# Kernel tuning notes

Measured on AMD Instinct MI355X. Metric: run time of the kernel, lower is better.

Reference implementation:

```python
import jax, jax.numpy as jnp
import numpy as np

EPS = 1e-12  # matches F.normalize default eps


def _l2norm(a, axis):
    n = jnp.sqrt(jnp.sum(a * a, axis=axis, keepdims=True))
    return a / jnp.maximum(n, EPS)


def setup_inputs() -> dict:
    key = jax.random.key(0)
    k1, k2, k3, k4, k5 = jax.random.split(key, 5)
    B, H, W = 512, 64, 64
    Y, Z = 32768, 1000
    x = jax.random.normal(k1, (B, H, W), dtype=jnp.float32)
    z = jax.random.randint(k2, (B,), 0, Z, dtype=jnp.int64 if jax.config.jax_enable_x64 else jnp.int32).astype(jnp.int32)
    x2y_w = jax.random.uniform(k3, (Y, H * W), dtype=jnp.float32)
    y2z_w = jax.random.uniform(k4, (Z, Y), dtype=jnp.float32)
    y_age = jax.random.randint(k5, (1, Y), 0, 3, dtype=jnp.int32)
    return {"x": x, "z": z, "x2y_w": x2y_w, "y2z_w": y2z_w, "y_age": y_age, "per_item": 1}


def reference(x, z, x2y_w, y2z_w, y_age, per_item):
    # DN.forward, mode='test'
    B = x.shape[0]
    Y = x2y_w.shape[0]
    xf = _l2norm(x.reshape(B, -1), axis=1)              # [B, X]
    w_xy = _l2norm(x2y_w, axis=1)                       # row-normalized [Y, X]
    w_yz = _l2norm(y2z_w, axis=1)                       # row-normalized [Z, Y]
    y_bu = jnp.einsum('bx,yx->by', xf, w_xy)            # bottom-up response [B, Y]
    active = (y_age >= 1).astype(y_bu.dtype)            # [1, Y] age gate
    y_pre = y_bu * active                               # gated responses
    # top_k_competition(flag=0): top-1 winner-take-all -> one-hot response
    winner = jnp.argmax(y_pre, axis=1)                  # [B]
    y_resp = jax.nn.one_hot(winner, Y, dtype=y_pre.dtype)  # [B, Y]
    out = jnp.einsum('by,zy->bz', y_resp, w_yz)         # [B, Z]
    return out
```

## Files before the change

### kernel.cpp

```cpp
#include <hip/hip_runtime.h>
#include <math.h>


typedef _Float16 half8 __attribute__((ext_vector_type(8)));
typedef __attribute__((ext_vector_type(16))) float f32x16;
typedef unsigned long long ull;

#define TAU 0.006f
#define CAP 1572864u
#define LCAP 1536u

__device__ __forceinline__ unsigned pk2h(float a, float b) {
    union { _Float16 h; unsigned short u; } ca, cb;
    ca.h = (_Float16)a; cb.h = (_Float16)b;
    return (unsigned)ca.u | ((unsigned)cb.u << 16);
}

__device__ __forceinline__ ull packkey(float v, unsigned y) {
    unsigned m = __float_as_uint(v);
    m = (v >= 0.f) ? (m | 0x80000000u) : ~m;
    return ((ull)m << 32) | (ull)(0x7FFFFFFFu - y);
}

__global__ __launch_bounds__(512) void init_ctrl(const int* __restrict__ age,
                                                 ull* __restrict__ win,
                                                 unsigned* __restrict__ cnt) {
    const int t = threadIdx.x;
    int fi = 0x7fffffff;
    for (int y = t; y < 32768; y += 512)
        if (age[y] < 1) fi = min(fi, y);
    __shared__ int red[512];
    red[t] = fi;
    __syncthreads();
    for (int s = 256; s; s >>= 1) {
        if (t < s) red[t] = min(red[t], red[t + s]);
        __syncthreads();
    }
    const int f = red[0];
    const ull seed = (f < 32768) ? packkey(0.0f, (unsigned)f) : packkey(-1e30f, 0u);
    win[t] = seed;
    if (t == 0) *cnt = 0u;
}

__global__ __launch_bounds__(512) void convert_x(const float* __restrict__ x,
                                                 uint4* __restrict__ xf16) {
    const int o = blockIdx.x * 512 + threadIdx.x;
    const int lane = o & 63;
    const int ks = (o >> 6) & 1;
    const int mi = (o >> 7) & 1;
    const int wm = (o >> 8) & 7;
    const int t  = o >> 11;
    const int row = (wm << 6) + (mi << 5) + (lane & 31);
    const int col = (t << 5) + (ks << 4) + ((lane >> 5) << 3);
    const float* src = x + (size_t)row * 4096 + col;
    const float4 a = *(const float4*)src;
    const float4 b = *(const float4*)(src + 4);
    uint4 u;
    u.x = pk2h(a.x, a.y); u.y = pk2h(a.z, a.w);
    u.z = pk2h(b.x, b.y); u.w = pk2h(b.z, b.w);
    xf16[o] = u;
}

__global__ __launch_bounds__(256) void row_norms(const float* __restrict__ src,
                                                 float* __restrict__ dst, int cols) {
    const int r = blockIdx.x;
    const float* row = src + (size_t)r * cols;
    const int t = threadIdx.x;
    float s = 0.f;
    const int nIter = cols >> 10;
    for (int i = 0; i < nIter; ++i) {
        const float4 v = *reinterpret_cast<const float4*>(row + (((i << 8) + t) << 2));
        s = fmaf(v.x, v.x, s); s = fmaf(v.y, v.y, s);
        s = fmaf(v.z, v.z, s); s = fmaf(v.w, v.w, s);
    }
    #pragma unroll
    for (int off = 32; off; off >>= 1) s += __shfl_down(s, off);
    __shared__ float red[4];
    if ((t & 63) == 0) red[t >> 6] = s;
    __syncthreads();
    if (t == 0) dst[r] = sqrtf(red[0] + red[1] + red[2] + red[3]);
}

__global__ __launch_bounds__(512, 2) void gemm_f16(
    const float* __restrict__ w,
    const uint4* __restrict__ xf16,
    const int*  __restrict__ age,
    float* __restrict__ cand,
    float2* __restrict__ ent,
    unsigned* __restrict__ cnt)
{
    __shared__ uint4 Bl[4][512];
    __shared__ float ny_inv[128];
    __shared__ float rowmaxs[512];
    __shared__ float2 lent[LCAP];
    __shared__ unsigned lcnt, gbase;

    const int tid = threadIdx.x;
    const int y0 = blockIdx.x << 7;

    const int rB = tid >> 2, q = tid & 3;
    const int wiB = (rB << 2) + (q ^ (rB & 3));
    const float* bP = w + (size_t)(y0 + rB) * 4096 + (q << 3);

    const int lane = tid & 63, wm = tid >> 6;
    const int kh = lane >> 5, cc = lane & 3;
    const uint4* aP = xf16 + (wm << 8) + lane;

    const int rb0 = ((lane & 31)      ) << 2;
    const int rb1 = ((lane & 31) +  32) << 2;
    const int rb2 = ((lane & 31) +  64) << 2;
    const int rb3 = ((lane & 31) +  96) << 2;
    const int s0 = kh ^ cc, s1 = (2 | kh) ^ cc;

    f32x16 am0n0 = (f32x16)0.f, am0n1 = (f32x16)0.f;
    f32x16 am0n2 = (f32x16)0.f, am0n3 = (f32x16)0.f;
    f32x16 am1n0 = (f32x16)0.f, am1n1 = (f32x16)0.f;
    f32x16 am1n2 = (f32x16)0.f, am1n3 = (f32x16)0.f;

    half8 pa00, pa01, pa10, pa11;
    half8 qa00, qa01, qa10, qa11;
    half8 g00, g10, g20, g30;
    half8 g01, g11, g21, g31;
    float4 SAa, SAb, SBa, SBb;
    float4 SCa, SCb, SDa, SDb;
    float nyacc = 0.f;

#define MF(a, b, c) __builtin_amdgcn_mfma_f32_32x32x16_f16(a, b, c, 0, 0, 0)
#define LG0 asm volatile("s_waitcnt lgkmcnt(0)" ::: "memory")
#define SBR __builtin_amdgcn_sched_barrier(0)

#define LOADA(S, tt) { const uint4* p_ = aP + ((size_t)(tt) << 11); \
    S##00 = *(const half8*)(p_);        S##01 = *(const half8*)(p_ + 64); \
    S##10 = *(const half8*)(p_ + 128);  S##11 = *(const half8*)(p_ + 192); }

#define LOADW(S, tt) { const float* p_ = bP + ((tt) << 5); \
    S##a = *(const float4*)p_; S##b = *(const float4*)(p_ + 4); }

#define STOREB(buf, S) { uint4 u_; \
    u_.x = pk2h(S##a.x, S##a.y); u_.y = pk2h(S##a.z, S##a.w); \
    u_.z = pk2h(S##b.x, S##b.y); u_.w = pk2h(S##b.z, S##b.w); \
    Bl[buf][wiB] = u_; \
    nyacc = fmaf(S##a.x, S##a.x, nyacc); nyacc = fmaf(S##a.y, S##a.y, nyacc); \
    nyacc = fmaf(S##a.z, S##a.z, nyacc); nyacc = fmaf(S##a.w, S##a.w, nyacc); \
    nyacc = fmaf(S##b.x, S##b.x, nyacc); nyacc = fmaf(S##b.y, S##b.y, nyacc); \
    nyacc = fmaf(S##b.z, S##b.z, nyacc); nyacc = fmaf(S##b.w, S##b.w, nyacc); }

#define LDB(cur) { \
    g00 = *(const half8*)&Bl[cur][rb0 + s0]; g01 = *(const half8*)&Bl[cur][rb0 + s1]; \
    g10 = *(const half8*)&Bl[cur][rb1 + s0]; g11 = *(const half8*)&Bl[cur][rb1 + s1]; \
    g20 = *(const half8*)&Bl[cur][rb2 + s0]; g21 = *(const half8*)&Bl[cur][rb2 + s1]; \
    g30 = *(const half8*)&Bl[cur][rb3 + s0]; g31 = *(const half8*)&Bl[cur][rb3 + s1]; }

#define MFMA16(S) { \
    am0n0 = MF(S##00, g00, am0n0); am0n1 = MF(S##00, g10, am0n1); \
    am0n2 = MF(S##00, g20, am0n2); am0n3 = MF(S##00, g30, am0n3); \
    am1n0 = MF(S##10, g00, am1n0); am1n1 = MF(S##10, g10, am1n1); \
    am1n2 = MF(S##10, g20, am1n2); am1n3 = MF(S##10, g30, am1n3); \
    am0n0 = MF(S##01, g01, am0n0); am0n1 = MF(S##01, g11, am0n1); \
    am0n2 = MF(S##01, g21, am0n2); am0n3 = MF(S##01, g31, am0n3); \
    am1n0 = MF(S##11, g01, am1n0); am1n1 = MF(S##11, g11, am1n1); \
    am1n2 = MF(S##11, g21, am1n2); am1n3 = MF(S##11, g31, am1n3); }

#define TILE(bR, bW, tt, AC, AN, WS, DOBAR) { \
    LDB(bR); \
    if ((tt) + 1 < 128) LOADA(AN, (tt) + 1); \
    if ((tt) + 2 < 128) STOREB(bW, WS); \
    if ((tt) + 6 < 128) LOADW(WS, (tt) + 6); \
    MFMA16(AC); \
    if (DOBAR) { LG0; SBR; __builtin_amdgcn_s_barrier(); } }

    LOADW(SA, 0); LOADW(SB, 1);
    LOADA(pa, 0);
    STOREB(0, SA);
    STOREB(1, SB);
    LOADW(SA, 2); LOADW(SB, 3); LOADW(SC, 4); LOADW(SD, 5);
    LG0; SBR;
    __builtin_amdgcn_s_barrier();

    for (int t = 0; t < 128; t += 4) {
        TILE(0, 2, t,     pa, qa, SA, 0)
        TILE(1, 3, t + 1, qa, pa, SB, 1)
        TILE(2, 0, t + 2, pa, qa, SC, 0)
        TILE(3, 1, t + 3, qa, pa, SD, 1)
    }

    float s_ = nyacc;
    s_ += __shfl_xor(s_, 1);
    s_ += __shfl_xor(s_, 2);
    if (q == 0) ny_inv[rB] = 1.0f / fmaxf(sqrtf(s_), 1e-12f);
    if (tid == 0) lcnt = 0u;
    __syncthreads();

    const int yl0 = (lane & 31), yl1 = yl0 + 32, yl2 = yl0 + 64, yl3 = yl0 + 96;
    const float scl0 = ny_inv[yl0], scl1 = ny_inv[yl1];
    const float scl2 = ny_inv[yl2], scl3 = ny_inv[yl3];
    const int act0 = age[y0 + yl0] >= 1, act1 = age[y0 + yl1] >= 1;
    const int act2 = age[y0 + yl2] >= 1, act3 = age[y0 + yl3] >= 1;
    const int yb0 = y0 + yl0, yb1 = y0 + yl1, yb2 = y0 + yl2, yb3 = y0 + yl3;
    const int rbase = (wm << 6) + (kh << 2);

#define ROWMAX(A0, A1, A2, A3, mi5) \
    _Pragma("unroll") for (int v = 0; v < 16; ++v) { \
        float bv = fmaxf( \
            fmaxf(act0 ? A0[v] * scl0 : 0.f, act1 ? A1[v] * scl1 : 0.f), \
            fmaxf(act2 ? A2[v] * scl2 : 0.f, act3 ? A3[v] * scl3 : 0.f)); \
        _Pragma("unroll") for (int off = 1; off < 32; off <<= 1) \
            bv = fmaxf(bv, __shfl_xor(bv, off)); \
        if ((lane & 31) == 0) \
            rowmaxs[rbase + (mi5) + (v & 3) + ((v >> 2) << 3)] = bv; \
    }
    ROWMAX(am0n0, am0n1, am0n2, am0n3, 0)
    ROWMAX(am1n0, am1n1, am1n2, am1n3, 32)
    __syncthreads();
    cand[(size_t)tid * 256 + blockIdx.x] = rowmaxs[tid];
    __syncthreads();

#define APP1(ACv, actk, sclk, ybk, r_) { \
    if (actk) { const float sc_ = (ACv) * sclk; \
        if (sc_ >= rowmaxs[r_] - TAU) { \
            const unsigned ix_ = atomicAdd(&lcnt, 1u); \
            if (ix_ < LCAP) lent[ix_] = make_float2(sc_, \
                __uint_as_float(((unsigned)(r_) << 16) | (unsigned)(ybk))); } } }

#define APPEND(A0, A1, A2, A3, mi5) \
    _Pragma("unroll") for (int v = 0; v < 16; ++v) { \
        const int r_ = rbase + (mi5) + (v & 3) + ((v >> 2) << 3); \
        APP1(A0[v], act0, scl0, yb0, r_) \
        APP1(A1[v], act1, scl1, yb1, r_) \
        APP1(A2[v], act2, scl2, yb2, r_) \
        APP1(A3[v], act3, scl3, yb3, r_) }
    APPEND(am0n0, am0n1, am0n2, am0n3, 0)
    APPEND(am1n0, am1n1, am1n2, am1n3, 32)
    __syncthreads();
    if (tid == 0) gbase = atomicAdd(cnt, min(lcnt, LCAP));
    __syncthreads();
    const unsigned nL = min(lcnt, LCAP);
    for (unsigned i = tid; i < nL; i += 512) {
        const unsigned gi = gbase + i;
        if (gi < CAP) ent[gi] = lent[i];
    }
#undef MF
#undef LG0
#undef SBR
#undef LOADA
#undef LOADW
#undef STOREB
#undef LDB
#undef MFMA16
#undef TILE
#undef ROWMAX
#undef APP1
#undef APPEND
}

__global__ __launch_bounds__(256) void reduce_gmax(const float* __restrict__ cand,
                                                   float* __restrict__ gmax) {
    const int b = blockIdx.x, t = threadIdx.x;
    float m = cand[(size_t)b * 256 + t];
    #pragma unroll
    for (int off = 32; off; off >>= 1) m = fmaxf(m, __shfl_xor(m, off));
    __shared__ float sm[4];
    if ((t & 63) == 0) sm[t >> 6] = m;
    __syncthreads();
    if (t == 0) gmax[b] = fmaxf(fmaxf(sm[0], sm[1]), fmaxf(sm[2], sm[3]));
}

__global__ __launch_bounds__(256) void rescore(
    const float* __restrict__ x, const float* __restrict__ w,
    const float* __restrict__ gmax, const float2* __restrict__ ent,
    const unsigned* __restrict__ cnt, ull* __restrict__ win)
{
    const unsigned n = min(*cnt, CAP);
    const int lane = threadIdx.x & 63;
    const unsigned wid = (blockIdx.x * 256 + threadIdx.x) >> 6;
    const unsigned nwv = (gridDim.x * 256) >> 6;
    for (unsigned base = wid << 6; base < n; base += (nwv << 6)) {
        const unsigned e = base + (unsigned)lane;
        unsigned by = 0u;
        bool ok = false;
        if (e < n) {
            const float2 en = ent[e];
            by = __float_as_uint(en.y);
            ok = en.x >= gmax[by >> 16] - TAU;
        }
        ull m = __ballot(ok);
        while (m) {
            const int s = __ffsll((ull)m) - 1;
            m &= m - 1;
            const unsigned bys = __shfl(by, s);
            const unsigned b = bys >> 16, y = bys & 0xffffu;
            const float4* xr = (const float4*)(x + (size_t)b * 4096);
            const float4* wr = (const float4*)(w + (size_t)y * 4096);
            float sdot = 0.f, nn = 0.f;
            #pragma unroll
            for (int k = 0; k < 16; ++k) {
                const float4 xv = xr[(k << 6) + lane];
                const float4 wv = wr[(k << 6) + lane];
                sdot = fmaf(xv.x, wv.x, sdot); sdot = fmaf(xv.y, wv.y, sdot);
                sdot = fmaf(xv.z, wv.z, sdot); sdot = fmaf(xv.w, wv.w, sdot);
                nn = fmaf(wv.x, wv.x, nn); nn = fmaf(wv.y, wv.y, nn);
                nn = fmaf(wv.z, wv.z, nn); nn = fmaf(wv.w, wv.w, nn);
            }
            #pragma unroll
            for (int off = 32; off; off >>= 1) {
                sdot += __shfl_xor(sdot, off);
                nn   += __shfl_xor(nn, off);
            }
            if (lane == 0) {
                const float sc = sdot / fmaxf(sqrtf(nn), 1e-12f);
                atomicMax(win + b, packkey(sc, y));
            }
        }
    }
}

__global__ __launch_bounds__(256) void gather_out(const float* __restrict__ y2z,
                                                  const float* __restrict__ nz,
                                                  const ull* __restrict__ win,
                                                  float* __restrict__ out) {
    const int g = blockIdx.x * 256 + threadIdx.x;
    if (g >= 512 * 1000) return;
    const int b = g / 1000, z = g - b * 1000;
    const unsigned lo = (unsigned)(win[b] & 0xffffffffull);
    const int yw = (int)(0x7FFFFFFFu - lo);
    out[g] = y2z[(size_t)z * 32768 + yw] / fmaxf(nz[z], 1e-12f);
}

extern "C" void kernel_launch(void* const* d_in, const int* in_sizes, int n_in,
                              void* d_out, int out_size, void* d_ws, size_t ws_size,
                              hipStream_t stream) {
    const float* x     = (const float*)d_in[0];
    const float* x2y_w = (const float*)d_in[2];
    const float* y2z_w = (const float*)d_in[3];
    const int*   y_age = (const int*)d_in[4];
    float* out = (float*)d_out;

    char* p = (char*)d_ws;
    float*    cand = (float*)p;
    float*    nz   = (float*)(p + 524288);
    float*    gmax = (float*)(p + 528384);
    ull*      win  = (ull*)(p + 530432);
    unsigned* cnt  = (unsigned*)(p + 534528);
    uint4*    xf16 = (uint4*)(p + 534592);
    float2*   ent  = (float2*)(p + 4728896);

    init_ctrl<<<1, 512, 0, stream>>>(y_age, win, cnt);
    convert_x<<<512, 512, 0, stream>>>(x, xf16);
    row_norms<<<1000, 256, 0, stream>>>(y2z_w, nz, 32768);

    gemm_f16<<<256, 512, 0, stream>>>(x2y_w, xf16, y_age, cand, ent, cnt);
    reduce_gmax<<<512, 256, 0, stream>>>(cand, gmax);
    rescore<<<256, 256, 0, stream>>>(x, x2y_w, gmax, ent, cnt, win);
    gather_out<<<(512 * 1000 + 255) / 256, 256, 0, stream>>>(y2z_w, nz, win, out);
}
```

Before: 311.1 us.

## Load weight rows in 64-byte nontemporal chunks covering two K-tiles per stage

Each thread now loads 16 contiguous fp32 weights per stage using nontemporal loads and writes two fp16 tiles into paired LDS buffers, so each prefetch stage covers two K-tiles. The main loop is restructured around 64 stages with a barrier after every tile instead of every other tile. The aim is wider, streaming global reads of the large weight matrix without polluting cache. The cost is more barriers and fewer prefetch stages in flight, which shortens the prefetch lead.

```diff
diff --git a/kernel.cpp b/kernel.cpp
--- a/kernel.cpp
+++ b/kernel.cpp
@@ -4,6 +4,7 @@
 
 typedef _Float16 half8 __attribute__((ext_vector_type(8)));
 typedef __attribute__((ext_vector_type(16))) float f32x16;
+typedef float f32x4 __attribute__((ext_vector_type(4)));
 typedef unsigned long long ull;
 
 #define TAU 0.006f
@@ -99,8 +100,10 @@
     const int y0 = blockIdx.x << 7;
 
     const int rB = tid >> 2, q = tid & 3;
-    const int wiB = (rB << 2) + (q ^ (rB & 3));
-    const float* bP = w + (size_t)(y0 + rB) * 4096 + (q << 3);
+    const int sb = (q & 1) << 1;
+    const int wi0 = (rB << 2) + ((sb    ) ^ (rB & 3));
+    const int wi1 = (rB << 2) + ((sb | 1) ^ (rB & 3));
+    const float* bP = w + (size_t)(y0 + rB) * 4096 + (q << 4);
 
     const int lane = tid & 63, wm = tid >> 6;
     const int kh = lane >> 5, cc = lane & 3;
@@ -121,29 +124,40 @@
     half8 qa00, qa01, qa10, qa11;
     half8 g00, g10, g20, g30;
     half8 g01, g11, g21, g31;
-    float4 SAa, SAb, SBa, SBb;
-    float4 SCa, SCb, SDa, SDb;
+    f32x4 SAa, SAb, SAc, SAd;
+    f32x4 SBa, SBb, SBc, SBd;
     float nyacc = 0.f;
 
 #define MF(a, b, c) __builtin_amdgcn_mfma_f32_32x32x16_f16(a, b, c, 0, 0, 0)
 #define LG0 asm volatile("s_waitcnt lgkmcnt(0)" ::: "memory")
 #define SBR __builtin_amdgcn_sched_barrier(0)
+#define BAR __builtin_amdgcn_s_barrier()
 
 #define LOADA(S, tt) { const uint4* p_ = aP + ((size_t)(tt) << 11); \
     S##00 = *(const half8*)(p_);        S##01 = *(const half8*)(p_ + 64); \
     S##10 = *(const half8*)(p_ + 128);  S##11 = *(const half8*)(p_ + 192); }
 
-#define LOADW(S, tt) { const float* p_ = bP + ((tt) << 5); \
-    S##a = *(const float4*)p_; S##b = *(const float4*)(p_ + 4); }
-
-#define STOREB(buf, S) { uint4 u_; \
-    u_.x = pk2h(S##a.x, S##a.y); u_.y = pk2h(S##a.z, S##a.w); \
-    u_.z = pk2h(S##b.x, S##b.y); u_.w = pk2h(S##b.z, S##b.w); \
-    Bl[buf][wiB] = u_; \
+#define LOADW(S, st) { const f32x4* p_ = (const f32x4*)(bP + ((st) << 6)); \
+    S##a = __builtin_nontemporal_load(p_); \
+    S##b = __builtin_nontemporal_load(p_ + 1); \
+    S##c = __builtin_nontemporal_load(p_ + 2); \
+    S##d = __builtin_nontemporal_load(p_ + 3); }
+
+#define STOREB2(bufE, bufO, S) { uint4 u0_, u1_; \
+    u0_.x = pk2h(S##a.x, S##a.y); u0_.y = pk2h(S##a.z, S##a.w); \
+    u0_.z = pk2h(S##b.x, S##b.y); u0_.w = pk2h(S##b.z, S##b.w); \
+    u1_.x = pk2h(S##c.x, S##c.y); u1_.y = pk2h(S##c.z, S##c.w); \
+    u1_.z = pk2h(S##d.x, S##d.y); u1_.w = pk2h(S##d.z, S##d.w); \
+    uint4* dst_ = (q < 2) ? Bl[bufE] : Bl[bufO]; \
+    dst_[wi0] = u0_; dst_[wi1] = u1_; \
     nyacc = fmaf(S##a.x, S##a.x, nyacc); nyacc = fmaf(S##a.y, S##a.y, nyacc); \
     nyacc = fmaf(S##a.z, S##a.z, nyacc); nyacc = fmaf(S##a.w, S##a.w, nyacc); \
     nyacc = fmaf(S##b.x, S##b.x, nyacc); nyacc = fmaf(S##b.y, S##b.y, nyacc); \
-    nyacc = fmaf(S##b.z, S##b.z, nyacc); nyacc = fmaf(S##b.w, S##b.w, nyacc); }
+    nyacc = fmaf(S##b.z, S##b.z, nyacc); nyacc = fmaf(S##b.w, S##b.w, nyacc); \
+    nyacc = fmaf(S##c.x, S##c.x, nyacc); nyacc = fmaf(S##c.y, S##c.y, nyacc); \
+    nyacc = fmaf(S##c.z, S##c.z, nyacc); nyacc = fmaf(S##c.w, S##c.w, nyacc); \
+    nyacc = fmaf(S##d.x, S##d.x, nyacc); nyacc = fmaf(S##d.y, S##d.y, nyacc); \
+    nyacc = fmaf(S##d.z, S##d.z, nyacc); nyacc = fmaf(S##d.w, S##d.w, nyacc); }
 
 #define LDB(cur) { \
     g00 = *(const half8*)&Bl[cur][rb0 + s0]; g01 = *(const half8*)&Bl[cur][rb0 + s1]; \
@@ -161,27 +175,27 @@
     am1n0 = MF(S##11, g01, am1n0); am1n1 = MF(S##11, g11, am1n1); \
     am1n2 = MF(S##11, g21, am1n2); am1n3 = MF(S##11, g31, am1n3); }
 
-#define TILE(bR, bW, tt, AC, AN, WS, DOBAR) { \
-    LDB(bR); \
-    if ((tt) + 1 < 128) LOADA(AN, (tt) + 1); \
-    if ((tt) + 2 < 128) STOREB(bW, WS); \
-    if ((tt) + 6 < 128) LOADW(WS, (tt) + 6); \
-    MFMA16(AC); \
-    if (DOBAR) { LG0; SBR; __builtin_amdgcn_s_barrier(); } }
-
-    LOADW(SA, 0); LOADW(SB, 1);
+    LOADW(SA, 0);
     LOADA(pa, 0);
-    STOREB(0, SA);
-    STOREB(1, SB);
-    LOADW(SA, 2); LOADW(SB, 3); LOADW(SC, 4); LOADW(SD, 5);
-    LG0; SBR;
-    __builtin_amdgcn_s_barrier();
-
-    for (int t = 0; t < 128; t += 4) {
-        TILE(0, 2, t,     pa, qa, SA, 0)
-        TILE(1, 3, t + 1, qa, pa, SB, 1)
-        TILE(2, 0, t + 2, pa, qa, SC, 0)
-        TILE(3, 1, t + 3, qa, pa, SD, 1)
+    STOREB2(0, 1, SA);
+    LOADW(SB, 1);
+    LOADW(SA, 2);
+    LG0; SBR; BAR;
+
+    for (int s = 0; s < 64; s += 2) {
+        const int t0 = s << 1;
+        LDB(0); LOADA(qa, t0 + 1);
+        STOREB2(2, 3, SB);
+        if (s + 3 < 64) LOADW(SB, s + 3);
+        MFMA16(pa); LG0; SBR; BAR;
+        LDB(1); LOADA(pa, t0 + 2);
+        MFMA16(qa); LG0; SBR; BAR;
+        LDB(2); LOADA(qa, t0 + 3);
+        if (s + 2 < 64) STOREB2(0, 1, SA);
+        if (s + 4 < 64) LOADW(SA, s + 4);
+        MFMA16(pa); LG0; SBR; BAR;
+        LDB(3); if (t0 + 4 < 128) LOADA(pa, t0 + 4);
+        MFMA16(qa); LG0; SBR; BAR;
     }
 
     float s_ = nyacc;
@@ -242,12 +256,12 @@
 #undef MF
 #undef LG0
 #undef SBR
+#undef BAR
 #undef LOADA
 #undef LOADW
-#undef STOREB
+#undef STOREB2
 #undef LDB
 #undef MFMA16
-#undef TILE
 #undef ROWMAX
 #undef APP1
 #undef APPEND
```

Result: slower. 352.1 us (+13.2%).
